# Kernel tuning notes

Hardware: AMD Instinct MI355X
Metric: run time of the kernel (lower is better)

The kernel has to match this reference:

```python
import jax, jax.numpy as jnp
import numpy as np

TAU = 0.2
ALPHA = 0.8
EPS = 1e-8  # torch cosine_similarity eps
LAM_POS = 1.5  # generate_lambda()=0.5, +1 for extrapolation
LAM_NEG = 0.5  # interpolation lambda


def _cos_sim_matrix(x):
    # row-normalize with clamped norm (matches F.cosine_similarity eps), then gram matrix
    n = x / jnp.maximum(jnp.linalg.norm(x, axis=1, keepdims=True), EPS)
    return n @ n.T


def setup_inputs() -> dict:
    key = jax.random.key(0)
    N, D = 4096, 512
    emb = jax.random.normal(key, (N, D), dtype=jnp.float32)
    # SimCLR-style symmetric positive pairs: (2k,2k+1) and (2k+1,2k)
    base = np.arange(0, N, 2)
    fwd_pairs = np.stack([base, base + 1], axis=1)
    pairs = np.concatenate([fwd_pairs, fwd_pairs[:, ::-1]], axis=0)  # [N, 2]
    return {"embeddings": emb, "positive_pairs": jnp.asarray(pairs, dtype=jnp.int32)}


def reference(embeddings, positive_pairs):
    # stage == 'train' (quantile-thresholded hard-negative branch)
    N = embeddings.shape[0]
    ar = jnp.arange(N)
    pi, pj = positive_pairs[:, 0], positive_pairs[:, 1]
    # ordered positive mask (symmetric because pairs include both orientations)
    pos_mask = jnp.zeros((N, N), dtype=bool).at[pi, pj].set(True)

    # --- extrapolate positive pairs: row i -> 1.5*e_i - 0.5*e_j ---
    partner_pos = jnp.full((N,), -1, dtype=jnp.int32).at[pi].set(pj.astype(jnp.int32))
    in_pair = partner_pos >= 0
    pp = jnp.where(in_pair, partner_pos, 0)
    hard_pos_emb = jnp.where(
        in_pair[:, None],
        LAM_POS * embeddings - (LAM_POS - 1.0) * embeddings[pp],
        embeddings,
    )

    # --- interpolate negative pairs: row k -> 0.5*(e_k + e_partner) ---
    # Negative pairs are all ordered (i,j), i!=j, not positive, scattered in
    # row k is the largest i with (i,k) negative.
    valid = (~pos_mask.T) & (ar[None, :] != ar[:, None])  # valid[k, i] = (i,k) is negative
    partner_neg = jnp.max(jnp.where(valid, ar[None, :], -1), axis=1)
    hard_neg_emb = LAM_NEG * embeddings + (1.0 - LAM_NEG) * embeddings[partner_neg]

    # --- three NxN cosine-sim matrices, composed by the scatter pattern ---
    orig_sim = _cos_sim_matrix(embeddings)
    hard_pos_sim = _cos_sim_matrix(hard_pos_emb)
    hard_neg_sim = _cos_sim_matrix(hard_neg_emb)
    diag = jnp.eye(N, dtype=bool)
    sim = jnp.where(diag, orig_sim, jnp.where(pos_mask, hard_pos_sim, hard_neg_sim))

    # --- contrastive loss with per-row quantile hard-negative threshold ---
    mask = diag | pos_mask
    exp_sim = jnp.exp(sim / TAU)
    exp_masked = jnp.where(mask, 0.0, exp_sim)
    pos_sim = exp_sim[pi, pj]              # [P]
    exp_rows = exp_masked[pi]              # [P, N]
    thr = jnp.quantile(exp_rows, ALPHA, axis=1, keepdims=True)
    hard_neg_sum = jnp.sum(jnp.where(exp_rows >= thr, exp_rows, 0.0), axis=1)
    loss = -jnp.log(pos_sim / (pos_sim + hard_neg_sum))
    # torch sums loss_ij + loss_ji over all rows / (2*P); with symmetric pair
    # list this equals sum(loss_ij)/P
    return jnp.sum(loss) / positive_pairs.shape[0]
```

## Files before the change

kernel.cpp:

```cpp
#include <hip/hip_runtime.h>
#include <cmath>

#define DIM 512
#define TAU_INV 5.0f
#define EPSN 1e-8f
#define ALPHA_Q 0.8f
#define TPITCH 72

typedef __attribute__((ext_vector_type(8))) unsigned short us8;
typedef __attribute__((ext_vector_type(4))) unsigned short us4;
typedef __attribute__((ext_vector_type(8))) short s8v;
typedef __attribute__((ext_vector_type(4))) float f4;

__device__ __forceinline__ unsigned short f2h(float f) {
    _Float16 h = (_Float16)f;
    return *(const unsigned short*)&h;
}
__device__ __forceinline__ float h2f(unsigned u) {
    unsigned short us = (unsigned short)u;
    _Float16 h = *(const _Float16*)&us;
    return (float)h;
}
__device__ __forceinline__ unsigned key16(unsigned u) {
    return u ^ (0x8000u | (0x7FFFu & (0u - (u >> 15))));
}
__device__ __forceinline__ float keyval(unsigned k) {
    unsigned u = (k & 0x8000u) ? (k & 0x7FFFu) : ((~k) & 0xFFFFu);
    return h2f(u);
}

__global__ void k_scatter(const int* __restrict__ pairs, int* partner, int P) {
    int k = blockIdx.x * 256 + threadIdx.x;
    if (k < P) partner[pairs[2 * k]] = pairs[2 * k + 1];
}

__global__ __launch_bounds__(64) void k_prep(const float* __restrict__ emb,
                                             const int* __restrict__ partner,
                                             const int* __restrict__ pairs,
                                             unsigned short* __restrict__ mb,
                                             float* __restrict__ pos_term,
                                             int N, int P) {
    int bid = blockIdx.x, t = threadIdx.x;
    if (bid < N) {
        int i = bid;
        int q = N - 1;
        if (q == i || partner[q] == i) q = N - 2;
        if (q == i || partner[q] == i) q = N - 3;
        const float4* A = (const float4*)(emb + (size_t)i * DIM);
        const float4* B = (const float4*)(emb + (size_t)q * DIM);
        float4 a0 = A[t], a1 = A[t + 64];
        float4 b0 = B[t], b1 = B[t + 64];
        float h0x = 0.5f * (a0.x + b0.x), h0y = 0.5f * (a0.y + b0.y);
        float h0z = 0.5f * (a0.z + b0.z), h0w = 0.5f * (a0.w + b0.w);
        float h1x = 0.5f * (a1.x + b1.x), h1y = 0.5f * (a1.y + b1.y);
        float h1z = 0.5f * (a1.z + b1.z), h1w = 0.5f * (a1.w + b1.w);
        float ss = h0x * h0x + h0y * h0y + h0z * h0z + h0w * h0w
                 + h1x * h1x + h1y * h1y + h1z * h1z + h1w * h1w;
        for (int o = 32; o > 0; o >>= 1) ss += __shfl_xor(ss, o);
        float inv = 1.0f / fmaxf(sqrtf(ss), EPSN);
        us4 lo, hi;
        lo[0] = f2h(h0x * inv); lo[1] = f2h(h0y * inv);
        lo[2] = f2h(h0z * inv); lo[3] = f2h(h0w * inv);
        hi[0] = f2h(h1x * inv); hi[1] = f2h(h1y * inv);
        hi[2] = f2h(h1z * inv); hi[3] = f2h(h1w * inv);
        *(us4*)(mb + (size_t)i * DIM + t * 4) = lo;
        *(us4*)(mb + (size_t)i * DIM + 256 + t * 4) = hi;
    } else {
        int k = bid - N;
        int i = pairs[2 * k], j = pairs[2 * k + 1];
        const float4* A = (const float4*)(emb + (size_t)i * DIM);
        const float4* B = (const float4*)(emb + (size_t)j * DIM);
        float4 a0 = A[t], a1 = A[t + 64];
        float4 b0 = B[t], b1 = B[t + 64];
        float dab = 0.f, naa = 0.f, nbb = 0.f;
        float fa, fb;
        fa = 1.5f * a0.x - 0.5f * b0.x; fb = 1.5f * b0.x - 0.5f * a0.x; dab += fa * fb; naa += fa * fa; nbb += fb * fb;
        fa = 1.5f * a0.y - 0.5f * b0.y; fb = 1.5f * b0.y - 0.5f * a0.y; dab += fa * fb; naa += fa * fa; nbb += fb * fb;
        fa = 1.5f * a0.z - 0.5f * b0.z; fb = 1.5f * b0.z - 0.5f * a0.z; dab += fa * fb; naa += fa * fa; nbb += fb * fb;
        fa = 1.5f * a0.w - 0.5f * b0.w; fb = 1.5f * b0.w - 0.5f * a0.w; dab += fa * fb; naa += fa * fa; nbb += fb * fb;
        fa = 1.5f * a1.x - 0.5f * b1.x; fb = 1.5f * b1.x - 0.5f * a1.x; dab += fa * fb; naa += fa * fa; nbb += fb * fb;
        fa = 1.5f * a1.y - 0.5f * b1.y; fb = 1.5f * b1.y - 0.5f * a1.y; dab += fa * fb; naa += fa * fa; nbb += fb * fb;
        fa = 1.5f * a1.z - 0.5f * b1.z; fb = 1.5f * b1.z - 0.5f * a1.z; dab += fa * fb; naa += fa * fa; nbb += fb * fb;
        fa = 1.5f * a1.w - 0.5f * b1.w; fb = 1.5f * b1.w - 0.5f * a1.w; dab += fa * fb; naa += fa * fa; nbb += fb * fb;
        for (int o = 32; o > 0; o >>= 1) {
            dab += __shfl_xor(dab, o);
            naa += __shfl_xor(naa, o);
            nbb += __shfl_xor(nbb, o);
        }
        if (t == 0) {
            float sim = dab / (fmaxf(sqrtf(naa), EPSN) * fmaxf(sqrtf(nbb), EPSN));
            pos_term[k] = expf(sim * TAU_INV);
        }
    }
}

__global__ __launch_bounds__(256, 3) void k_gemm_sym(const unsigned short* __restrict__ mb,
                                                     unsigned short* __restrict__ S, int N) {
    __shared__ __align__(16) unsigned short smem[4 * 64 * TPITCH];
    int tid = threadIdx.x;
    int wave = tid >> 6, lane = tid & 63, quad = lane >> 4, l16 = lane & 15;
    int wr = (wave >> 1) * 64, wc = (wave & 1) * 64;

    int ntb = N >> 7;
    int bi = 0, rem = blockIdx.x, rowlen = ntb;
    while (rem >= rowlen) { rem -= rowlen; ++bi; --rowlen; }
    int bj = bi + rem;
    int iBase = bi * 128, jBase = bj * 128;
    int lrow = lane >> 2, lseg = lane & 3;

    const unsigned short* gA0 = mb + (size_t)(iBase + wave * 32 + lrow) * DIM + lseg * 8;
    const unsigned short* gA1 = gA0 + 16 * DIM;
    const unsigned short* gB0 = mb + (size_t)(jBase + wave * 32 + lrow) * DIM + lseg * 8;
    const unsigned short* gB1 = gB0 + 16 * DIM;

    __attribute__((address_space(3))) char* ldsBase =
        (__attribute__((address_space(3))) char*)smem;
    __attribute__((address_space(3))) char* ldsA0 = ldsBase + wave * 2048;
    __attribute__((address_space(3))) char* ldsA1 = ldsBase + 8192 + wave * 2048;
    __attribute__((address_space(3))) char* ldsB0 = ldsBase + 16384 + wave * 2048;
    __attribute__((address_space(3))) char* ldsB1 = ldsBase + 24576 + wave * 2048;

    f4 acc[4][4];
    for (int i = 0; i < 4; ++i)
        for (int j = 0; j < 4; ++j) acc[i][j] = (f4){0.f, 0.f, 0.f, 0.f};

    for (int k0 = 0; k0 < DIM; k0 += 64) {
        __syncthreads();
        __builtin_amdgcn_global_load_lds(
            (const __attribute__((address_space(1))) void*)(gA0 + k0),
            (__attribute__((address_space(3))) void*)(ldsA0), 16, 0, 0);
        __builtin_amdgcn_global_load_lds(
            (const __attribute__((address_space(1))) void*)(gA1 + k0),
            (__attribute__((address_space(3))) void*)(ldsA0 + 1024), 16, 0, 0);
        __builtin_amdgcn_global_load_lds(
            (const __attribute__((address_space(1))) void*)(gA0 + k0 + 32),
            (__attribute__((address_space(3))) void*)(ldsA1), 16, 0, 0);
        __builtin_amdgcn_global_load_lds(
            (const __attribute__((address_space(1))) void*)(gA1 + k0 + 32),
            (__attribute__((address_space(3))) void*)(ldsA1 + 1024), 16, 0, 0);
        __builtin_amdgcn_global_load_lds(
            (const __attribute__((address_space(1))) void*)(gB0 + k0),
            (__attribute__((address_space(3))) void*)(ldsB0), 16, 0, 0);
        __builtin_amdgcn_global_load_lds(
            (const __attribute__((address_space(1))) void*)(gB1 + k0),
            (__attribute__((address_space(3))) void*)(ldsB0 + 1024), 16, 0, 0);
        __builtin_amdgcn_global_load_lds(
            (const __attribute__((address_space(1))) void*)(gB0 + k0 + 32),
            (__attribute__((address_space(3))) void*)(ldsB1), 16, 0, 0);
        __builtin_amdgcn_global_load_lds(
            (const __attribute__((address_space(1))) void*)(gB1 + k0 + 32),
            (__attribute__((address_space(3))) void*)(ldsB1 + 1024), 16, 0, 0);
        __syncthreads();

        #pragma unroll
        for (int h = 0; h < 2; ++h) {
            s8v a[4], b[4];
            #pragma unroll
            for (int i = 0; i < 4; ++i)
                a[i] = *(const s8v*)&smem[h * 4096 + (wr + i * 16 + l16) * 32 + quad * 8];
            #pragma unroll
            for (int j = 0; j < 4; ++j)
                b[j] = *(const s8v*)&smem[8192 + h * 4096 + (wc + j * 16 + l16) * 32 + quad * 8];
            #pragma unroll
            for (int i = 0; i < 4; ++i)
                #pragma unroll
                for (int j = 0; j < 4; ++j)
                    acc[i][j] = __builtin_amdgcn_mfma_f32_16x16x32_f16(a[i], b[j], acc[i][j], 0, 0, 0);
        }
    }
    int rQ = iBase + wr + quad * 4;
    int cQ = jBase + wc + l16;
    for (int i = 0; i < 4; ++i)
        for (int j = 0; j < 4; ++j)
            for (int rr = 0; rr < 4; ++rr)
                S[(size_t)(rQ + i * 16 + rr) * N + cQ + j * 16] = f2h(acc[i][j][rr]);

    if (bi != bj) {
        __syncthreads();
        unsigned short* T = smem + wave * 64 * TPITCH;
        #pragma unroll
        for (int i = 0; i < 4; ++i)
            #pragma unroll
            for (int j = 0; j < 4; ++j)
                #pragma unroll
                for (int rr = 0; rr < 4; ++rr) {
                    int tr = quad * 4 + i * 16 + rr;
                    int tc = l16 + j * 16;
                    T[tc * TPITCH + tr] = f2h(acc[i][j][rr]);
                }
        int lrow8 = lane >> 3, lseg8 = lane & 7;
        #pragma unroll
        for (int it = 0; it < 8; ++it) {
            int mr = it * 8 + lrow8;
            us8 v = *(const us8*)&T[mr * TPITCH + lseg8 * 8];
            *(us8*)&S[(size_t)(jBase + wc + mr) * N + iBase + wr + lseg8 * 8] = v;
        }
    }
}

__global__ __launch_bounds__(256) void k_gemm(const unsigned short* __restrict__ mb,
                                              unsigned short* __restrict__ S, int N, int rowBase) {
    __shared__ __align__(16) unsigned short As[128][32];
    __shared__ __align__(16) unsigned short Bs[128][32];
    int tid = threadIdx.x;
    int wave = tid >> 6, lane = tid & 63, quad = lane >> 4, l16 = lane & 15;
    int wr = (wave >> 1) * 64, wc = (wave & 1) * 64;
    int iBase = rowBase + blockIdx.y * 128;
    int jBase = blockIdx.x * 128;
    int lrow = lane >> 2, lseg = lane & 3;

    const unsigned short* gA0 = mb + (size_t)(iBase + wave * 32 + lrow) * DIM + lseg * 8;
    const unsigned short* gA1 = gA0 + 16 * DIM;
    const unsigned short* gB0 = mb + (size_t)(jBase + wave * 32 + lrow) * DIM + lseg * 8;
    const unsigned short* gB1 = gB0 + 16 * DIM;
    __attribute__((address_space(3))) char* ldsA =
        (__attribute__((address_space(3))) char*)As + wave * 2048;
    __attribute__((address_space(3))) char* ldsB =
        (__attribute__((address_space(3))) char*)Bs + wave * 2048;

    f4 acc[4][4];
    for (int i = 0; i < 4; ++i)
        for (int j = 0; j < 4; ++j) acc[i][j] = (f4){0.f, 0.f, 0.f, 0.f};

    for (int k0 = 0; k0 < DIM; k0 += 32) {
        __syncthreads();
        __builtin_amdgcn_global_load_lds(
            (const __attribute__((address_space(1))) void*)(gA0 + k0),
            (__attribute__((address_space(3))) void*)(ldsA), 16, 0, 0);
        __builtin_amdgcn_global_load_lds(
            (const __attribute__((address_space(1))) void*)(gA1 + k0),
            (__attribute__((address_space(3))) void*)(ldsA + 1024), 16, 0, 0);
        __builtin_amdgcn_global_load_lds(
            (const __attribute__((address_space(1))) void*)(gB0 + k0),
            (__attribute__((address_space(3))) void*)(ldsB), 16, 0, 0);
        __builtin_amdgcn_global_load_lds(
            (const __attribute__((address_space(1))) void*)(gB1 + k0),
            (__attribute__((address_space(3))) void*)(ldsB + 1024), 16, 0, 0);
        __syncthreads();

        s8v a[4], b[4];
        for (int i = 0; i < 4; ++i) a[i] = *(const s8v*)&As[wr + i * 16 + l16][quad * 8];
        for (int j = 0; j < 4; ++j) b[j] = *(const s8v*)&Bs[wc + j * 16 + l16][quad * 8];
        for (int i = 0; i < 4; ++i)
            for (int j = 0; j < 4; ++j)
                acc[i][j] = __builtin_amdgcn_mfma_f32_16x16x32_f16(a[i], b[j], acc[i][j], 0, 0, 0);
    }
    int rQ = blockIdx.y * 128 + wr + quad * 4;
    int cQ = jBase + wc + l16;
    for (int i = 0; i < 4; ++i)
        for (int j = 0; j < 4; ++j)
            for (int rr = 0; rr < 4; ++rr)
                S[(size_t)(rQ + i * 16 + rr) * N + cQ + j * 16] = f2h(acc[i][j][rr]);
}

__global__ __launch_bounds__(128, 4) void k_select(const unsigned short* __restrict__ Sb,
                                                   const int* __restrict__ pairs,
                                                   const float* __restrict__ pos_term,
                                                   float* __restrict__ losses,
                                                   int N, int r0, int r1, int P,
                                                   int klo, float frac) {
    int wid = threadIdx.x >> 6, lane = threadIdx.x & 63;
    int k = blockIdx.x * 2 + wid;
    if (k >= P) return;
    int row = pairs[2 * k];
    if (row < r0 || row >= r1) return;
    int pj = pairs[2 * k + 1];
    const us8* src8 = (const us8*)(Sb + (size_t)(row - r0) * N);

    unsigned kr[32];
    #pragma unroll
    for (int t = 0; t < 8; ++t)
        *(us8*)&kr[t * 4] = src8[t * 64 + lane];

    #pragma unroll
    for (int t = 0; t < 8; ++t) {
        int j0 = (t * 64 + lane) * 8;
        #pragma unroll
        for (int m = 0; m < 4; ++m) {
            unsigned p = kr[t * 4 + m];
            unsigned lo = key16(p & 0xFFFFu);
            unsigned hi = key16(p >> 16);
            int jlo = j0 + 2 * m, jhi = jlo + 1;
            if (jlo == row || jlo == pj) lo = 0u;
            if (jhi == row || jhi == pj) hi = 0u;
            kr[t * 4 + m] = lo | (hi << 16);
        }
    }

    int nmask = (pj == row) ? 1 : 2;
    int Nreal = N - nmask;
    int Rreal = klo - nmask;
    float pos = pos_term[k];
    float s = 0.f;

    if (Rreal < 0) {
        #pragma unroll
        for (int i = 0; i < 32; ++i) {
            unsigned lo = kr[i] & 0xFFFFu, hi = kr[i] >> 16;
            if (lo > 0u) s += __expf(keyval(lo) * TAU_INV);
            if (hi > 0u) s += __expf(keyval(hi) * TAU_INV);
        }
    } else {
        int lim = Nreal - Rreal - 1;
        unsigned lo_ = 1, hi_ = 65535;
        while (lo_ < hi_) {
            unsigned mid = (lo_ + hi_) >> 1;
            unsigned cnt = 0;
            #pragma unroll
            for (int i = 0; i < 32; ++i) {
                cnt += (unsigned)__popcll(__ballot((kr[i] & 0xFFFFu) > mid));
                cnt += (unsigned)__popcll(__ballot((kr[i] >> 16) > mid));
            }
            if (cnt <= (unsigned)lim) hi_ = mid; else lo_ = mid + 1;
        }
        unsigned K1 = lo_;

        if (frac > 1e-9f) {
            unsigned cntAbove = 0, mymin = 0xFFFFFFFFu;
            #pragma unroll
            for (int i = 0; i < 32; ++i) {
                unsigned lo = kr[i] & 0xFFFFu, hi = kr[i] >> 16;
                bool glo = lo > K1, ghi = hi > K1;
                cntAbove += (unsigned)__popcll(__ballot(glo));
                cntAbove += (unsigned)__popcll(__ballot(ghi));
                if (glo && lo < mymin) mymin = lo;
                if (ghi && hi < mymin) mymin = hi;
            }
            for (int o = 1; o < 64; o <<= 1) {
                unsigned y = (unsigned)__shfl_xor((int)mymin, o);
                if (y < mymin) mymin = y;
            }
            unsigned K2;
            if (Rreal + 1 > Nreal - 1)                   K2 = K1;
            else if (Nreal - (int)cntAbove >= Rreal + 2) K2 = K1;
            else                                         K2 = mymin;
            float elo = __expf(keyval(K1) * TAU_INV);
            float ehi = __expf(keyval(K2) * TAU_INV);
            float thr = elo + frac * (ehi - elo);
            #pragma unroll
            for (int i = 0; i < 32; ++i) {
                unsigned lo = kr[i] & 0xFFFFu, hi = kr[i] >> 16;
                if (lo > 0u) { float ev = __expf(keyval(lo) * TAU_INV); if (ev >= thr) s += ev; }
                if (hi > 0u) { float ev = __expf(keyval(hi) * TAU_INV); if (ev >= thr) s += ev; }
            }
        } else {
            #pragma unroll
            for (int i = 0; i < 32; ++i) {
                unsigned lo = kr[i] & 0xFFFFu, hi = kr[i] >> 16;
                if (lo >= K1) s += __expf(keyval(lo) * TAU_INV);
                if (hi >= K1) s += __expf(keyval(hi) * TAU_INV);
            }
        }
    }

    for (int o = 1; o < 64; o <<= 1) s += __shfl_xor(s, o);
    if (lane == 0) losses[k] = logf((pos + s) / pos);
}

__global__ __launch_bounds__(256) void k_reduce(const float* __restrict__ losses,
                                                float* __restrict__ out, int P, float invP) {
    __shared__ float s_red[4];
    int tid = threadIdx.x, wid = tid >> 6, lane = tid & 63;
    float s = 0.f;
    for (int i = tid; i < P; i += 256) s += losses[i];
    for (int o = 1; o < 64; o <<= 1) s += __shfl_xor(s, o);
    if (lane == 0) s_red[wid] = s;
    __syncthreads();
    if (tid == 0) out[0] = (s_red[0] + s_red[1] + s_red[2] + s_red[3]) * invP;
}

extern "C" void kernel_launch(void* const* d_in, const int* in_sizes, int n_in,
                              void* d_out, int out_size, void* d_ws, size_t ws_size,
                              hipStream_t stream) {
    const float* emb = (const float*)d_in[0];
    const int* pairs = (const int*)d_in[1];
    float* out = (float*)d_out;
    int N = in_sizes[0] / DIM;
    int P = in_sizes[1] / 2;

    char* ws = (char*)d_ws;
    size_t off = 0;
    unsigned short* mb = (unsigned short*)(ws + off); off += (size_t)N * DIM * 2;
    int* partner = (int*)(ws + off);                  off += (size_t)N * 4;
    float* pos_term = (float*)(ws + off);             off += (size_t)P * 4;
    float* losses = (float*)(ws + off);               off += (size_t)P * 4;
    off = (off + 255) & ~(size_t)255;
    unsigned short* Sbuf = (unsigned short*)(ws + off);
    size_t avail = (ws_size > off) ? ws_size - off : 0;
    long maxRows = (long)(avail / ((size_t)N * 2));
    int chunk = (int)(maxRows - (maxRows % 128));
    if (chunk > N) chunk = N;
    if (chunk < 128) chunk = 128;

    k_scatter<<<dim3((P + 255) / 256), dim3(256), 0, stream>>>(pairs, partner, P);
    k_prep<<<dim3(N + P), dim3(64), 0, stream>>>(emb, partner, pairs, mb, pos_term, N, P);

    float qpos = ALPHA_Q * (float)(N - 1);
    int klo = (int)floorf(qpos);
    float frac = qpos - (float)klo;
    float invP = 1.0f / (float)P;

    if (chunk >= N) {
        int ntb = N >> 7;
        int nblk = ntb * (ntb + 1) / 2;
        k_gemm_sym<<<dim3(nblk), dim3(256), 0, stream>>>(mb, Sbuf, N);
        k_select<<<dim3((P + 1) / 2), dim3(128), 0, stream>>>(Sbuf, pairs, pos_term, losses,
                                                              N, 0, N, P, klo, frac);
    } else {
        for (int r0 = 0; r0 < N; r0 += chunk) {
            int rows = (N - r0 < chunk) ? (N - r0) : chunk;
            dim3 g(N / 128, rows / 128);
            k_gemm<<<g, dim3(256), 0, stream>>>(mb, Sbuf, N, r0);
            k_select<<<dim3((P + 1) / 2), dim3(128), 0, stream>>>(Sbuf, pairs, pos_term, losses,
                                                                  N, r0, r0 + rows, P, klo, frac);
        }
    }
    k_reduce<<<dim3(1), dim3(256), 0, stream>>>(losses, out, P, invP);
}
```

Baseline: 122.4 us.

## Double-buffer LDS tiles in Gram GEMM to overlap loads with MFMA

Replaces the load-sync-compute loop over 64-wide K chunks with a two-buffer pipeline over 32-wide chunks. The next chunk is prefetched into the alternate LDS buffer via global_load_lds while MFMAs run on the current buffer, with one barrier per step. The aim is to hide global-to-LDS latency behind compute. The cost is twice as many iterations and barriers, each doing half the MFMA work. The barrier before the transpose epilogue is dropped because the loop now ends with one.

```diff
diff --git a/kernel.cpp b/kernel.cpp
--- a/kernel.cpp
+++ b/kernel.cpp
@@ -115,59 +115,52 @@
 
     __attribute__((address_space(3))) char* ldsBase =
         (__attribute__((address_space(3))) char*)smem;
-    __attribute__((address_space(3))) char* ldsA0 = ldsBase + wave * 2048;
-    __attribute__((address_space(3))) char* ldsA1 = ldsBase + 8192 + wave * 2048;
-    __attribute__((address_space(3))) char* ldsB0 = ldsBase + 16384 + wave * 2048;
-    __attribute__((address_space(3))) char* ldsB1 = ldsBase + 24576 + wave * 2048;
+
+#define STAGE(buf, koff)                                                                   \
+    do {                                                                                   \
+        __attribute__((address_space(3))) char* dA = ldsBase + (buf) * 16384 + wave * 2048;\
+        __attribute__((address_space(3))) char* dB = dA + 8192;                            \
+        __builtin_amdgcn_global_load_lds(                                                  \
+            (const __attribute__((address_space(1))) void*)(gA0 + (koff)),                 \
+            (__attribute__((address_space(3))) void*)(dA), 16, 0, 0);                      \
+        __builtin_amdgcn_global_load_lds(                                                  \
+            (const __attribute__((address_space(1))) void*)(gA1 + (koff)),                 \
+            (__attribute__((address_space(3))) void*)(dA + 1024), 16, 0, 0);               \
+        __builtin_amdgcn_global_load_lds(                                                  \
+            (const __attribute__((address_space(1))) void*)(gB0 + (koff)),                 \
+            (__attribute__((address_space(3))) void*)(dB), 16, 0, 0);                      \
+        __builtin_amdgcn_global_load_lds(                                                  \
+            (const __attribute__((address_space(1))) void*)(gB1 + (koff)),                 \
+            (__attribute__((address_space(3))) void*)(dB + 1024), 16, 0, 0);               \
+    } while (0)
 
     f4 acc[4][4];
     for (int i = 0; i < 4; ++i)
         for (int j = 0; j < 4; ++j) acc[i][j] = (f4){0.f, 0.f, 0.f, 0.f};
 
-    for (int k0 = 0; k0 < DIM; k0 += 64) {
+    STAGE(0, 0);
+    __syncthreads();
+    int cur = 0;
+    for (int t = 0; t < 16; ++t) {
+        if (t < 15) STAGE(cur ^ 1, (t + 1) * 32);
+        const unsigned short* base = smem + cur * 8192;
+        s8v a[4], b[4];
+        #pragma unroll
+        for (int i = 0; i < 4; ++i)
+            a[i] = *(const s8v*)&base[(wr + i * 16 + l16) * 32 + quad * 8];
+        #pragma unroll
+        for (int j = 0; j < 4; ++j)
+            b[j] = *(const s8v*)&base[4096 + (wc + j * 16 + l16) * 32 + quad * 8];
+        #pragma unroll
+        for (int i = 0; i < 4; ++i)
+            #pragma unroll
+            for (int j = 0; j < 4; ++j)
+                acc[i][j] = __builtin_amdgcn_mfma_f32_16x16x32_f16(a[i], b[j], acc[i][j], 0, 0, 0);
         __syncthreads();
-        __builtin_amdgcn_global_load_lds(
-            (const __attribute__((address_space(1))) void*)(gA0 + k0),
-            (__attribute__((address_space(3))) void*)(ldsA0), 16, 0, 0);
-        __builtin_amdgcn_global_load_lds(
-            (const __attribute__((address_space(1))) void*)(gA1 + k0),
-            (__attribute__((address_space(3))) void*)(ldsA0 + 1024), 16, 0, 0);
-        __builtin_amdgcn_global_load_lds(
-            (const __attribute__((address_space(1))) void*)(gA0 + k0 + 32),
-            (__attribute__((address_space(3))) void*)(ldsA1), 16, 0, 0);
-        __builtin_amdgcn_global_load_lds(
-            (const __attribute__((address_space(1))) void*)(gA1 + k0 + 32),
-            (__attribute__((address_space(3))) void*)(ldsA1 + 1024), 16, 0, 0);
-        __builtin_amdgcn_global_load_lds(
-            (const __attribute__((address_space(1))) void*)(gB0 + k0),
-            (__attribute__((address_space(3))) void*)(ldsB0), 16, 0, 0);
-        __builtin_amdgcn_global_load_lds(
-            (const __attribute__((address_space(1))) void*)(gB1 + k0),
-            (__attribute__((address_space(3))) void*)(ldsB0 + 1024), 16, 0, 0);
-        __builtin_amdgcn_global_load_lds(
-            (const __attribute__((address_space(1))) void*)(gB0 + k0 + 32),
-            (__attribute__((address_space(3))) void*)(ldsB1), 16, 0, 0);
-        __builtin_amdgcn_global_load_lds(
-            (const __attribute__((address_space(1))) void*)(gB1 + k0 + 32),
-            (__attribute__((address_space(3))) void*)(ldsB1 + 1024), 16, 0, 0);
-        __syncthreads();
-
-        #pragma unroll
-        for (int h = 0; h < 2; ++h) {
-            s8v a[4], b[4];
-            #pragma unroll
-            for (int i = 0; i < 4; ++i)
-                a[i] = *(const s8v*)&smem[h * 4096 + (wr + i * 16 + l16) * 32 + quad * 8];
-            #pragma unroll
-            for (int j = 0; j < 4; ++j)
-                b[j] = *(const s8v*)&smem[8192 + h * 4096 + (wc + j * 16 + l16) * 32 + quad * 8];
-            #pragma unroll
-            for (int i = 0; i < 4; ++i)
-                #pragma unroll
-                for (int j = 0; j < 4; ++j)
-                    acc[i][j] = __builtin_amdgcn_mfma_f32_16x16x32_f16(a[i], b[j], acc[i][j], 0, 0, 0);
-        }
-    }
+        cur ^= 1;
+    }
+#undef STAGE
+
     int rQ = iBase + wr + quad * 4;
     int cQ = jBase + wc + l16;
     for (int i = 0; i < 4; ++i)
@@ -176,7 +169,6 @@
                 S[(size_t)(rQ + i * 16 + rr) * N + cQ + j * 16] = f2h(acc[i][j][rr]);
 
     if (bi != bj) {
-        __syncthreads();
         unsigned short* T = smem + wave * 64 * TPITCH;
         #pragma unroll
         for (int i = 0; i < 4; ++i)
```

Result: no change. 121.3 us (-0.9%).
